# Performance work log

Measured on AMD Instinct MI355X. Metric: run time of the kernel, lower is better.

The kernel has to match this reference:

```python
import jax, jax.numpy as jnp
import numpy as np

# ---- config (from init_kwargs) ----
PRE_NMS_THRESH = 0.05
K = 200                    # pre_nms_top_n (fixed-size top-k for jit)
NUM_CLASSES = 80
FPN_STRIDE = 8
MASK_SCALE_FACTOR = 2
MASK_STRIDE = FPN_STRIDE / MASK_SCALE_FACTOR  # 4.0
IMG_H, IMG_W = 768, 768


def setup_inputs() -> dict:
    key = jax.random.key(0)
    ks = jax.random.split(key, 6)
    N, C, H, W, DIM = 2, NUM_CLASSES, 96, 96, 32
    # FCOS-style locations for the stride-8 level: center of each cell
    ys, xs = jnp.meshgrid(jnp.arange(H, dtype=jnp.float32),
                          jnp.arange(W, dtype=jnp.float32), indexing='ij')
    locations = jnp.stack([xs.reshape(-1), ys.reshape(-1)], axis=1) * FPN_STRIDE + FPN_STRIDE // 2
    return {
        'locations': locations,                                                 # [HW, 2]
        'box_cls': jax.random.normal(ks[0], (N, C, H, W), jnp.float32) - 2.0,   # mostly below thresh
        'box_regression': jax.random.uniform(ks[1], (N, 4, H, W), jnp.float32) * 100.0,
        'centerness': jax.random.normal(ks[2], (N, 1, H, W), jnp.float32),
        'proposal_embed': jax.random.normal(ks[3], (N, DIM, H, W), jnp.float32),
        'proposal_margin': jax.random.uniform(ks[4], (N, 1, H, W), jnp.float32, minval=0.1, maxval=2.0),
        'pixel_embed': jax.random.normal(ks[5], (N, DIM, 192, 192), jnp.float32),
    }


def reference(locations, box_cls, box_regression, centerness,
              proposal_embed, proposal_margin, pixel_embed):
    N, C, H, W = box_cls.shape
    DIM = proposal_embed.shape[1]
    o_h = pixel_embed.shape[2] * MASK_SCALE_FACTOR
    o_w = pixel_embed.shape[3] * MASK_SCALE_FACTOR

    # interpolate(pixel_embed, size=(o_h, o_w), mode='bilinear', align_corners=False)
    pix_up = jax.image.resize(pixel_embed, (N, DIM, o_h, o_w), method='bilinear')

    # NCHW -> [N, HW, C] flattening (matches permute(0,2,3,1).reshape)
    scores = jax.nn.sigmoid(jnp.transpose(box_cls.reshape(N, C, H * W), (0, 2, 1)))   # [N, HW, C]
    ctr = jax.nn.sigmoid(centerness.reshape(N, H * W))                                # [N, HW]
    reg = jnp.transpose(box_regression.reshape(N, 4, H * W), (0, 2, 1))               # [N, HW, 4]
    emb = jnp.transpose(proposal_embed.reshape(N, DIM, H * W), (0, 2, 1))             # [N, HW, DIM]
    mar = proposal_margin.reshape(N, H * W)                                           # [N, HW]

    xs = jnp.arange(o_w, dtype=jnp.float32)
    ys = jnp.arange(o_h, dtype=jnp.float32)

    def per_image(s, c, r, e, m, pix):
        # threshold + centerness-weighted score; invalid candidates rank last
        cand = s > PRE_NMS_THRESH                       # [HW, C]
        sc = s * c[:, None]                             # [HW, C]
        flat = jnp.where(cand, sc, -1.0).reshape(-1)    # [HW*C]
        topv, topi = jax.lax.top_k(flat, K)             # fixed-size top-k
        loc_idx = topi // C                             # [K]
        labels = topi % C + 1                           # [K]
        valid = topv > 0.0                              # padded slots when < K candidates

        # box decode: [x - l, y - t, x + r, y + b], clipped to image
        loc = locations[loc_idx]                        # [K, 2]
        rr = r[loc_idx]                                 # [K, 4]
        x1 = jnp.clip(loc[:, 0] - rr[:, 0], 0.0, IMG_W - 1)
        y1 = jnp.clip(loc[:, 1] - rr[:, 1], 0.0, IMG_H - 1)
        x2 = jnp.clip(loc[:, 0] + rr[:, 2], 0.0, IMG_W - 1)
        y2 = jnp.clip(loc[:, 1] + rr[:, 3], 0.0, IMG_H - 1)
        boxes = jnp.stack([x1, y1, x2, y2], axis=1)     # [K, 4]

        # boxes_to_masks at mask stride: binary inside-box masks [K, o_h, o_w]
        mb = boxes / MASK_STRIDE
        in_x = (xs[None, :] >= mb[:, 0:1]) & (xs[None, :] <= mb[:, 2:3])  # [K, o_w]
        in_y = (ys[None, :] >= mb[:, 1:2]) & (ys[None, :] <= mb[:, 3:4])  # [K, o_h]
        box_mask = in_y[:, :, None] & in_x[:, None, :]

        # pixel-embed distance mask: exp(-||pix - e_k||^2 * margin_k)
        ek = e[loc_idx]                                 # [K, DIM]
        mk = m[loc_idx]                                 # [K]
        p = pix.reshape(DIM, o_h * o_w)                 # [DIM, P]
        d2 = (jnp.sum(ek * ek, axis=1)[:, None]
              + jnp.sum(p * p, axis=0)[None, :]
              - 2.0 * ek @ p)                           # [K, P] via GEMM
        prob = jnp.exp(-d2 * mk[:, None]).reshape(K, o_h, o_w)
        masks = prob * box_mask.astype(prob.dtype) * valid[:, None, None].astype(prob.dtype)
        return masks

    masks = jax.vmap(per_image)(scores, ctr, reg, emb, mar, pix_up)  # [N, K, o_h, o_w]
    return masks
```

## Files before the change

kernel.cpp:

```cpp
#include <hip/hip_runtime.h>
#include <cmath>


namespace {
constexpr int NIMG = 2;
constexpr int NC   = 80;
constexpr int NHW  = 96 * 96;
constexpr int NCHW = NC * NHW;
constexpr int NDIM = 32;
constexpr int PH = 192, PW = 192;
constexpr int OH = 384, OW = 384;
constexpr int KTOP = 200;
constexpr int CAP = 4096;
constexpr int MCAP = 1024;
constexpr float PRE_THRESH = 0.05f;
constexpr unsigned KEY_ZERO = 0x80000000u;
constexpr float IMG_MAX = 767.0f;

constexpr int ZTILES = 6;
constexpr int NZB = NIMG * KTOP * ZTILES;

constexpr int NF4 = NCHW / 4;
constexpr int SEL_BLOCKS = 128;
constexpr int SEL_STRIDE = SEL_BLOCKS * 256;
constexpr int SEL_ITERS = (NF4 + SEL_STRIDE - 1) / SEL_STRIDE;
constexpr int LCAP = 512;

constexpr int WS_HIST1  = 0;
constexpr int WS_CNT    = WS_HIST1 + NIMG * 2048;
constexpr int WS_PAIRS  = 4104;
constexpr int WS_PARAMS = WS_PAIRS + NIMG * CAP * 2;
constexpr int PARAM_WORDS = 40;
constexpr int WS_ZERO_WORDS = WS_CNT + NIMG;

typedef float f4 __attribute__((ext_vector_type(4)));
}

__device__ __forceinline__ unsigned key_of(float f) {
  unsigned u = __float_as_uint(f);
  return (u & 0x80000000u) ? ~u : (u | 0x80000000u);
}

__device__ void scan2048(const unsigned* __restrict__ gh, int kwant,
                         unsigned* sh_cnt, unsigned* sh_sum, int* sh_bk,
                         int& b_out, int& kr_out) {
  const int t = threadIdx.x;
  __syncthreads();
  if (t == 0) { sh_bk[0] = -1; sh_bk[1] = kwant; }
  unsigned local = 0;
  for (int j = 0; j < 8; ++j) { unsigned v = gh[t * 8 + j]; sh_cnt[t * 8 + j] = v; local += v; }
  sh_sum[t] = local;
  __syncthreads();
  unsigned S = 0;
  for (int j = t + 1; j < 256; ++j) S += sh_sum[j];
  int cand_b = -1;
  unsigned cand_above = 0;
  unsigned run = S;
  for (int j = 7; j >= 0; --j) {
    const unsigned cv = sh_cnt[t * 8 + j];
    if (cand_b < 0 && run + cv >= (unsigned)kwant) { cand_b = t * 8 + j; cand_above = run; }
    run += cv;
  }
  if (cand_b >= 0) atomicMax(&sh_bk[0], cand_b);
  __syncthreads();
  if (cand_b >= 0 && cand_b == sh_bk[0]) sh_bk[1] = kwant - (int)cand_above;
  __syncthreads();
  b_out = (sh_bk[0] < 0) ? 0 : sh_bk[0];
  kr_out = sh_bk[1];
}

__global__ __launch_bounds__(256) void k_zero_ws(unsigned* __restrict__ ws) {
  const int i = blockIdx.x * 256 + threadIdx.x;
  for (int j = i; j < WS_ZERO_WORDS; j += 8 * 256) ws[j] = 0u;
}

__global__ __launch_bounds__(256) void k_keygen(const float* __restrict__ box_cls,
                                                const float* __restrict__ ctrness,
                                                unsigned* __restrict__ ws,
                                                uint4* __restrict__ keys) {
  __shared__ unsigned hist[2048];
  for (int i = threadIdx.x; i < 2048; i += 256) hist[i] = 0;
  __syncthreads();
  const int n = blockIdx.x >= SEL_BLOCKS;
  const int bi = blockIdx.x - n * SEL_BLOCKS;
  const float* cls = box_cls + n * NCHW;
  const float* ctr = ctrness + n * NHW;
  uint4* mykeys = keys + n * NF4;
  for (int s = 0; s < SEL_ITERS; ++s) {
    const int j4 = s * SEL_STRIDE + bi * 256 + threadIdx.x;
    if (j4 >= NF4) break;
    const int j = j4 * 4;
    const int c = j / NHW;
    const int hw = j - c * NHW;
    const f4 xv = *reinterpret_cast<const f4*>(cls + j);
    const f4 cv = *reinterpret_cast<const f4*>(ctr + hw);
    unsigned kk[4];
    #pragma unroll
    for (int q = 0; q < 4; ++q) {
      const float sg = 1.0f / (1.0f + expf(-xv[q]));
      float v = -1.0f;
      if (sg > PRE_THRESH) v = sg * (1.0f / (1.0f + expf(-cv[q])));
      const unsigned k = key_of(v);
      kk[q] = k;
      if (k > KEY_ZERO) atomicAdd(&hist[k >> 21], 1u);
    }
    mykeys[j4] = make_uint4(kk[0], kk[1], kk[2], kk[3]);
  }
  __syncthreads();
  unsigned* gh = ws + WS_HIST1 + n * 2048;
  for (int t = threadIdx.x; t < 2048; t += 256) { unsigned v = hist[t]; if (v) atomicAdd(&gh[t], v); }
}

__global__ __launch_bounds__(256) void k_gather(const uint4* __restrict__ keys,
                                                unsigned* __restrict__ ws) {
  __shared__ unsigned sh_cnt[2048];
  __shared__ unsigned sh_sum[256];
  __shared__ int sh_bk[2];
  __shared__ unsigned loc[LCAP][2];
  __shared__ int lcnt;
  __shared__ unsigned gbase;
  const int n = blockIdx.x >= SEL_BLOCKS;
  const int bi = blockIdx.x - n * SEL_BLOCKS;
  int b1i, kr;
  scan2048(ws + WS_HIST1 + n * 2048, KTOP, sh_cnt, sh_sum, sh_bk, b1i, kr);
  if (threadIdx.x == 0) lcnt = 0;
  __syncthreads();
  const unsigned b1 = (unsigned)b1i;
  const uint4* mykeys = keys + n * NF4;
  for (int s = 0; s < SEL_ITERS; ++s) {
    const int j4 = s * SEL_STRIDE + bi * 256 + threadIdx.x;
    if (j4 >= NF4) break;
    const uint4 kv = mykeys[j4];
    const unsigned kk[4] = {kv.x, kv.y, kv.z, kv.w};
    #pragma unroll
    for (int q = 0; q < 4; ++q) {
      if ((kk[q] >> 21) < b1) continue;
      const int j = j4 * 4 + q;
      const int c = j / NHW;
      const int hw = j - c * NHW;
      const int p = atomicAdd(&lcnt, 1);
      if (p < LCAP) { loc[p][0] = kk[q]; loc[p][1] = (unsigned)(hw * NC + c); }
    }
  }
  __syncthreads();
  const int lc = min(lcnt, LCAP);
  if (threadIdx.x == 0) gbase = atomicAdd(ws + WS_CNT + n, (unsigned)lc);
  __syncthreads();
  const unsigned gb = gbase;
  for (int i = threadIdx.x; i < lc; i += 256) {
    const unsigned pos = gb + (unsigned)i;
    if (pos < (unsigned)CAP) {
      ws[WS_PAIRS + (n * CAP + (int)pos) * 2]     = loc[i][0];
      ws[WS_PAIRS + (n * CAP + (int)pos) * 2 + 1] = loc[i][1];
    }
  }
}

__global__ __launch_bounds__(256) void k_final(unsigned* __restrict__ ws,
                                               const float* __restrict__ locations,
                                               const float* __restrict__ box_reg,
                                               const float* __restrict__ pemb,
                                               const float* __restrict__ pmar) {
  const int n = blockIdx.x;
  const int t = threadIdx.x;
  __shared__ unsigned sh_cnt[2048];
  __shared__ unsigned sh_sum[256];
  __shared__ int sh_bk[2];
  __shared__ uint2 P[CAP];
  __shared__ unsigned h256[256];
  __shared__ unsigned mKey[MCAP], mRef[MCAP];
  __shared__ int sh_b, sh_t;
  for (int s = t; s < KTOP; s += 256) ws[WS_PARAMS + (n * KTOP + s) * PARAM_WORDS] = 0u;
  int b1i, krem;
  scan2048(ws + WS_HIST1 + n * 2048, KTOP, sh_cnt, sh_sum, sh_bk, b1i, krem);
  const unsigned b1 = (unsigned)b1i;
  const int cnt = min((int)ws[WS_CNT + n], CAP);
  for (int i = t; i < cnt; i += 256) {
    P[i].x = ws[WS_PAIRS + (n * CAP + i) * 2];
    P[i].y = ws[WS_PAIRS + (n * CAP + i) * 2 + 1];
  }
  __syncthreads();

  unsigned prefix = b1;
  int shift = 21;
  #pragma unroll
  for (int level = 0; level < 2; ++level) {
    const int newshift = shift - 8;
    h256[t] = 0;
    if (t == 0) sh_b = 0;
    __syncthreads();
    for (int i = t; i < cnt; i += 256) {
      const unsigned k = P[i].x;
      if ((k >> shift) == prefix) atomicAdd(&h256[(k >> newshift) & 255u], 1u);
    }
    __syncthreads();
    const unsigned hv = h256[t];
    unsigned S = 0;
    for (int j = t + 1; j < 256; ++j) S += h256[j];
    if (S + hv >= (unsigned)krem) atomicMax(&sh_b, t);
    __syncthreads();
    const int b = sh_b;
    if (t == b) sh_t = krem - (int)S;
    __syncthreads();
    krem = sh_t;
    prefix = (prefix << 8) | (unsigned)b;
    shift = newshift;
    __syncthreads();
  }

  if (t == 0) sh_t = 0;
  __syncthreads();
  for (int i = t; i < cnt; i += 256) {
    const unsigned k = P[i].x;
    if ((k >> 5) >= prefix) {
      const int pos = atomicAdd(&sh_t, 1);
      if (pos < MCAP) { mKey[pos] = k; mRef[pos] = P[i].y; }
    }
  }
  __syncthreads();
  const int m = min(sh_t, MCAP);

  for (int i = t; i < m; i += 256) {
    const unsigned ki = mKey[i], ri = mRef[i];
    int rank = 0;
    for (int j = 0; j < m; ++j) {
      const unsigned kj = mKey[j], rj = mRef[j];
      rank += (kj > ki || (kj == ki && rj < ri)) ? 1 : 0;
    }
    if (rank >= KTOP) continue;
    unsigned* pp = ws + WS_PARAMS + (n * KTOP + rank) * PARAM_WORDS;
    int valid = 0;
    if (ki > KEY_ZERO) {
      const int hw = (int)ri / NC;
      const float lx = locations[2 * hw], ly = locations[2 * hw + 1];
      const float rl = box_reg[(n * 4 + 0) * NHW + hw];
      const float rt = box_reg[(n * 4 + 1) * NHW + hw];
      const float rr = box_reg[(n * 4 + 2) * NHW + hw];
      const float rb = box_reg[(n * 4 + 3) * NHW + hw];
      const float x1 = fminf(fmaxf(lx - rl, 0.f), IMG_MAX);
      const float y1 = fminf(fmaxf(ly - rt, 0.f), IMG_MAX);
      const float x2 = fminf(fmaxf(lx + rr, 0.f), IMG_MAX);
      const float y2 = fminf(fmaxf(ly + rb, 0.f), IMG_MAX);
      const int ix0 = max(0, (int)ceilf(x1 * 0.25f));
      const int ix1 = min(OW - 1, (int)floorf(x2 * 0.25f));
      const int iy0 = max(0, (int)ceilf(y1 * 0.25f));
      const int iy1 = min(OH - 1, (int)floorf(y2 * 0.25f));
      if (ix0 <= ix1 && iy0 <= iy1) {
        valid = 1;
        pp[1] = (unsigned)ix0; pp[2] = (unsigned)ix1;
        pp[3] = (unsigned)iy0; pp[4] = (unsigned)iy1;
        reinterpret_cast<float*>(pp)[5] = pmar[n * NHW + hw];
        float* ep = reinterpret_cast<float*>(pp) + 8;
        #pragma unroll
        for (int d = 0; d < NDIM; ++d) ep[d] = pemb[(n * NDIM + d) * NHW + hw];
      }
    }
    pp[0] = (unsigned)valid;
  }
}

__global__ __launch_bounds__(256) void k_out(const float* __restrict__ pix,
                                             const unsigned* __restrict__ ws,
                                             float* __restrict__ out) {
  const int bid = blockIdx.x;
  const int t = threadIdx.x;
  if (bid < NZB) {
    const int nk = bid / ZTILES;
    const int rt = bid - nk * ZTILES;
    const int y0 = rt * 64;
    const unsigned* meta = ws + WS_PARAMS + nk * PARAM_WORDS;
    f4* ob4 = reinterpret_cast<f4*>(out + (size_t)nk * (OH * OW)) + y0 * (OW / 4);
    const f4 z = {0.f, 0.f, 0.f, 0.f};
    int qa = 0, qb = -1, iy0 = 0, iy1 = -1;
    bool overlap = false;
    if (meta[0]) {
      iy0 = (int)meta[3]; iy1 = (int)meta[4];
      if (iy1 >= y0 && iy0 < y0 + 64) {
        overlap = true;
        qa = (int)meta[1] >> 2;
        qb = (int)meta[2] >> 2;
      }
    }
    if (!overlap) {
      #pragma unroll
      for (int i = 0; i < 24; ++i) ob4[i * 256 + t] = z;
    } else {
      for (int i = 0; i < 24; ++i) {
        const int idx = i * 256 + t;
        const int y = y0 + idx / 96;
        const int q = idx - (idx / 96) * 96;
        if (y >= iy0 && y <= iy1 && q >= qa && q <= qb) continue;
        ob4[idx] = z;
      }
    }
    return;
  }

  const int nk = bid - NZB;
  const unsigned* meta = ws + WS_PARAMS + nk * PARAM_WORDS;
  if (meta[0] == 0u) return;
  const int ix0 = (int)meta[1], ix1 = (int)meta[2];
  const int iy0 = (int)meta[3], iy1 = (int)meta[4];
  const int xp0 = (ix0 >> 2) << 2;
  const int xp1 = (ix1 >> 2) * 4 + 3;
  const float margin = __uint_as_float(meta[5]);
  float e[NDIM];
  {
    const float4* e4 = reinterpret_cast<const float4*>(meta + 8);
    #pragma unroll
    for (int q = 0; q < NDIM / 4; ++q) {
      const float4 v = e4[q];
      e[4 * q + 0] = v.x; e[4 * q + 1] = v.y; e[4 * q + 2] = v.z; e[4 * q + 3] = v.w;
    }
  }
  const int n = nk / KTOP;
  const float* peb = pix + (size_t)n * NDIM * PH * PW;
  float* ob = out + (size_t)nk * (OH * OW);

  const int tx = t & 63;
  const int ts = t >> 6;
  const int h = iy1 - iy0 + 1;
  const int shh = (h + 3) >> 2;
  const int ybeg = iy0 + ts * shh;
  const int yend = min(iy0 + (ts + 1) * shh, iy1 + 1);

  for (int c = xp0 + tx; c <= xp1; c += 64) {
    const bool inx = (c >= ix0) && (c <= ix1);
    const float sx = 0.5f * (float)c - 0.25f;
    const float xf = floorf(sx);
    const float fx = sx - xf;
    const int xs0 = max((int)xf, 0);
    const int xs1 = min((int)xf + 1, PW - 1);
    float qa_[NDIM], qb_[NDIM];
    int ra = -9, rb = -9;
    for (int y = ybeg; y < yend; ++y) {
      float val = 0.f;
      if (inx) {
        const float sy = 0.5f * (float)y - 0.25f;
        const float yf = floorf(sy);
        const float fy = sy - yf;
        const int ys0 = max((int)yf, 0);
        const int ys1 = min((int)yf + 1, PH - 1);
        if (ys0 != ra) {
          if (ys0 == rb) {
            #pragma unroll
            for (int d = 0; d < NDIM; ++d) qa_[d] = qb_[d];
          } else {
            const float* p = peb + (size_t)ys0 * PW;
            #pragma unroll
            for (int d = 0; d < NDIM; ++d)
              qa_[d] = (1.f - fx) * p[d * PH * PW + xs0] + fx * p[d * PH * PW + xs1];
          }
          ra = ys0;
        }
        if (ys1 != rb) {
          if (ys1 == ra) {
            #pragma unroll
            for (int d = 0; d < NDIM; ++d) qb_[d] = qa_[d];
          } else {
            const float* p = peb + (size_t)ys1 * PW;
            #pragma unroll
            for (int d = 0; d < NDIM; ++d)
              qb_[d] = (1.f - fx) * p[d * PH * PW + xs0] + fx * p[d * PH * PW + xs1];
          }
          rb = ys1;
        }
        float d2 = 0.f;
        #pragma unroll
        for (int d = 0; d < NDIM; ++d) {
          const float pv = qa_[d] + fy * (qb_[d] - qa_[d]);
          const float df = e[d] - pv;
          d2 = fmaf(df, df, d2);
        }
        val = expf(-d2 * margin);
      }
      ob[(size_t)y * OW + c] = val;
    }
  }
}

extern "C" void kernel_launch(void* const* d_in, const int* in_sizes, int n_in,
                              void* d_out, int out_size, void* d_ws, size_t ws_size,
                              hipStream_t stream) {
  const float* locations = (const float*)d_in[0];
  const float* box_cls   = (const float*)d_in[1];
  const float* box_reg   = (const float*)d_in[2];
  const float* ctrness   = (const float*)d_in[3];
  const float* pemb      = (const float*)d_in[4];
  const float* pmar      = (const float*)d_in[5];
  const float* pix       = (const float*)d_in[6];
  float* out = (float*)d_out;
  unsigned* ws = (unsigned*)d_ws;
  uint4* keys = (uint4*)d_out;

  k_zero_ws<<<dim3(8), dim3(256), 0, stream>>>(ws);
  k_keygen <<<dim3(2 * SEL_BLOCKS), dim3(256), 0, stream>>>(box_cls, ctrness, ws, keys);
  k_gather <<<dim3(2 * SEL_BLOCKS), dim3(256), 0, stream>>>(keys, ws);
  k_final  <<<dim3(NIMG), dim3(256), 0, stream>>>(ws, locations, box_reg, pemb, pmar);
  k_out    <<<dim3(NZB + NIMG * KTOP), dim3(256), 0, stream>>>(pix, ws, out);
}
```

Before: 108.0 us.

## Fuse keygen, gather and final selection into one kernel with grid barrier

Merges the three selection kernels into a single persistent kernel. Score keys stay in registers instead of round-tripping through the output buffer. A global atomic spin barrier now separates the histogram from the gather, and a last-block ticket runs the final top-k and parameter packing. This removes two launches and the key store/reload, but relies on all 256 blocks being co-resident for the spin barrier. The output kernel is also reordered so the per-box compute blocks launch before the zero-fill blocks.

```diff
diff --git a/kernel.cpp b/kernel.cpp
--- a/kernel.cpp
+++ b/kernel.cpp
@@ -13,25 +13,28 @@
 constexpr int KTOP = 200;
 constexpr int CAP = 4096;
 constexpr int MCAP = 1024;
+constexpr int LCAP = 512;
 constexpr float PRE_THRESH = 0.05f;
 constexpr unsigned KEY_ZERO = 0x80000000u;
 constexpr float IMG_MAX = 767.0f;
 
+constexpr int NBOX = NIMG * KTOP;
 constexpr int ZTILES = 6;
-constexpr int NZB = NIMG * KTOP * ZTILES;
+constexpr int NZB = NBOX * ZTILES;
 
 constexpr int NF4 = NCHW / 4;
 constexpr int SEL_BLOCKS = 128;
 constexpr int SEL_STRIDE = SEL_BLOCKS * 256;
 constexpr int SEL_ITERS = (NF4 + SEL_STRIDE - 1) / SEL_STRIDE;
-constexpr int LCAP = 512;
 
 constexpr int WS_HIST1  = 0;
 constexpr int WS_CNT    = WS_HIST1 + NIMG * 2048;
+constexpr int WS_BAR    = WS_CNT + NIMG;
+constexpr int WS_TICK   = WS_BAR + 1;
+constexpr int WS_ZERO_WORDS = WS_TICK + NIMG;
 constexpr int WS_PAIRS  = 4104;
 constexpr int WS_PARAMS = WS_PAIRS + NIMG * CAP * 2;
 constexpr int PARAM_WORDS = 40;
-constexpr int WS_ZERO_WORDS = WS_CNT + NIMG;
 
 typedef float f4 __attribute__((ext_vector_type(4)));
 }
@@ -41,143 +44,146 @@
   return (u & 0x80000000u) ? ~u : (u | 0x80000000u);
 }
 
-__device__ void scan2048(const unsigned* __restrict__ gh, int kwant,
-                         unsigned* sh_cnt, unsigned* sh_sum, int* sh_bk,
-                         int& b_out, int& kr_out) {
-  const int t = threadIdx.x;
-  __syncthreads();
-  if (t == 0) { sh_bk[0] = -1; sh_bk[1] = kwant; }
-  unsigned local = 0;
-  for (int j = 0; j < 8; ++j) { unsigned v = gh[t * 8 + j]; sh_cnt[t * 8 + j] = v; local += v; }
-  sh_sum[t] = local;
-  __syncthreads();
-  unsigned S = 0;
-  for (int j = t + 1; j < 256; ++j) S += sh_sum[j];
-  int cand_b = -1;
-  unsigned cand_above = 0;
-  unsigned run = S;
-  for (int j = 7; j >= 0; --j) {
-    const unsigned cv = sh_cnt[t * 8 + j];
-    if (cand_b < 0 && run + cv >= (unsigned)kwant) { cand_b = t * 8 + j; cand_above = run; }
-    run += cv;
-  }
-  if (cand_b >= 0) atomicMax(&sh_bk[0], cand_b);
-  __syncthreads();
-  if (cand_b >= 0 && cand_b == sh_bk[0]) sh_bk[1] = kwant - (int)cand_above;
-  __syncthreads();
-  b_out = (sh_bk[0] < 0) ? 0 : sh_bk[0];
-  kr_out = sh_bk[1];
-}
-
 __global__ __launch_bounds__(256) void k_zero_ws(unsigned* __restrict__ ws) {
-  const int i = blockIdx.x * 256 + threadIdx.x;
-  for (int j = i; j < WS_ZERO_WORDS; j += 8 * 256) ws[j] = 0u;
-}
-
-__global__ __launch_bounds__(256) void k_keygen(const float* __restrict__ box_cls,
-                                                const float* __restrict__ ctrness,
-                                                unsigned* __restrict__ ws,
-                                                uint4* __restrict__ keys) {
+  for (int j = threadIdx.x; j < WS_ZERO_WORDS; j += 256) ws[j] = 0u;
+}
+
+__global__ __launch_bounds__(256) void k_select(
+    const float* __restrict__ box_cls, const float* __restrict__ ctrness,
+    const float* __restrict__ locations, const float* __restrict__ box_reg,
+    const float* __restrict__ pemb, const float* __restrict__ pmar,
+    unsigned* __restrict__ ws) {
   __shared__ unsigned hist[2048];
-  for (int i = threadIdx.x; i < 2048; i += 256) hist[i] = 0;
-  __syncthreads();
-  const int n = blockIdx.x >= SEL_BLOCKS;
-  const int bi = blockIdx.x - n * SEL_BLOCKS;
-  const float* cls = box_cls + n * NCHW;
-  const float* ctr = ctrness + n * NHW;
-  uint4* mykeys = keys + n * NF4;
-  for (int s = 0; s < SEL_ITERS; ++s) {
-    const int j4 = s * SEL_STRIDE + bi * 256 + threadIdx.x;
-    if (j4 >= NF4) break;
-    const int j = j4 * 4;
-    const int c = j / NHW;
-    const int hw = j - c * NHW;
-    const f4 xv = *reinterpret_cast<const f4*>(cls + j);
-    const f4 cv = *reinterpret_cast<const f4*>(ctr + hw);
-    unsigned kk[4];
-    #pragma unroll
-    for (int q = 0; q < 4; ++q) {
-      const float sg = 1.0f / (1.0f + expf(-xv[q]));
-      float v = -1.0f;
-      if (sg > PRE_THRESH) v = sg * (1.0f / (1.0f + expf(-cv[q])));
-      const unsigned k = key_of(v);
-      kk[q] = k;
-      if (k > KEY_ZERO) atomicAdd(&hist[k >> 21], 1u);
-    }
-    mykeys[j4] = make_uint4(kk[0], kk[1], kk[2], kk[3]);
-  }
-  __syncthreads();
-  unsigned* gh = ws + WS_HIST1 + n * 2048;
-  for (int t = threadIdx.x; t < 2048; t += 256) { unsigned v = hist[t]; if (v) atomicAdd(&gh[t], v); }
-}
-
-__global__ __launch_bounds__(256) void k_gather(const uint4* __restrict__ keys,
-                                                unsigned* __restrict__ ws) {
-  __shared__ unsigned sh_cnt[2048];
   __shared__ unsigned sh_sum[256];
   __shared__ int sh_bk[2];
   __shared__ unsigned loc[LCAP][2];
   __shared__ int lcnt;
   __shared__ unsigned gbase;
+  __shared__ int sh_last;
+  const int t = threadIdx.x;
   const int n = blockIdx.x >= SEL_BLOCKS;
   const int bi = blockIdx.x - n * SEL_BLOCKS;
-  int b1i, kr;
-  scan2048(ws + WS_HIST1 + n * 2048, KTOP, sh_cnt, sh_sum, sh_bk, b1i, kr);
-  if (threadIdx.x == 0) lcnt = 0;
-  __syncthreads();
-  const unsigned b1 = (unsigned)b1i;
-  const uint4* mykeys = keys + n * NF4;
+
+  for (int i = t; i < 2048; i += 256) hist[i] = 0;
+  __syncthreads();
+  const float* cls = box_cls + n * NCHW;
+  const float* ctr = ctrness + n * NHW;
+  unsigned kk[SEL_ITERS][4];
+  #pragma unroll
   for (int s = 0; s < SEL_ITERS; ++s) {
-    const int j4 = s * SEL_STRIDE + bi * 256 + threadIdx.x;
-    if (j4 >= NF4) break;
-    const uint4 kv = mykeys[j4];
-    const unsigned kk[4] = {kv.x, kv.y, kv.z, kv.w};
+    const int j4 = s * SEL_STRIDE + bi * 256 + t;
+    if (j4 < NF4) {
+      const int j = j4 * 4;
+      const int c = j / NHW;
+      const int hw = j - c * NHW;
+      const f4 xv = *reinterpret_cast<const f4*>(cls + j);
+      const f4 cv = *reinterpret_cast<const f4*>(ctr + hw);
+      #pragma unroll
+      for (int q = 0; q < 4; ++q) {
+        const float sg = 1.0f / (1.0f + expf(-xv[q]));
+        float v = -1.0f;
+        if (sg > PRE_THRESH) v = sg * (1.0f / (1.0f + expf(-cv[q])));
+        const unsigned k = key_of(v);
+        kk[s][q] = k;
+        if (k > KEY_ZERO) atomicAdd(&hist[k >> 21], 1u);
+      }
+    } else {
+      #pragma unroll
+      for (int q = 0; q < 4; ++q) kk[s][q] = 0u;
+    }
+  }
+  __syncthreads();
+  {
+    unsigned* gh = ws + WS_HIST1 + n * 2048;
+    for (int i = t; i < 2048; i += 256) { unsigned v = hist[i]; if (v) atomicAdd(&gh[i], v); }
+  }
+
+  __syncthreads();
+  if (t == 0) {
+    atomicAdd(ws + WS_BAR, 1u);
+    while (__hip_atomic_load(ws + WS_BAR, __ATOMIC_RELAXED,
+                             __HIP_MEMORY_SCOPE_AGENT) < (unsigned)(2 * SEL_BLOCKS)) {
+      __builtin_amdgcn_s_sleep(2);
+    }
+  }
+  __syncthreads();
+
+  if (t == 0) { sh_bk[0] = -1; sh_bk[1] = KTOP; }
+  {
+    const unsigned* gh = ws + WS_HIST1 + n * 2048;
+    unsigned local = 0;
+    for (int j = 0; j < 8; ++j) { unsigned v = gh[t * 8 + j]; hist[t * 8 + j] = v; local += v; }
+    sh_sum[t] = local;
+  }
+  __syncthreads();
+  {
+    unsigned S = 0;
+    for (int j = t + 1; j < 256; ++j) S += sh_sum[j];
+    int cand_b = -1;
+    unsigned cand_above = 0;
+    unsigned run = S;
+    for (int j = 7; j >= 0; --j) {
+      const unsigned cv = hist[t * 8 + j];
+      if (cand_b < 0 && run + cv >= (unsigned)KTOP) { cand_b = t * 8 + j; cand_above = run; }
+      run += cv;
+    }
+    if (cand_b >= 0) atomicMax(&sh_bk[0], cand_b);
+    __syncthreads();
+    if (cand_b >= 0 && cand_b == sh_bk[0]) sh_bk[1] = KTOP - (int)cand_above;
+    __syncthreads();
+  }
+  const unsigned b1 = (unsigned)(sh_bk[0] < 0 ? 0 : sh_bk[0]);
+  int krem = sh_bk[1];
+
+  if (t == 0) lcnt = 0;
+  __syncthreads();
+  #pragma unroll
+  for (int s = 0; s < SEL_ITERS; ++s) {
     #pragma unroll
     for (int q = 0; q < 4; ++q) {
-      if ((kk[q] >> 21) < b1) continue;
-      const int j = j4 * 4 + q;
+      const unsigned k = kk[s][q];
+      if ((k >> 21) < b1) continue;
+      const int j = (s * SEL_STRIDE + bi * 256 + t) * 4 + q;
       const int c = j / NHW;
       const int hw = j - c * NHW;
       const int p = atomicAdd(&lcnt, 1);
-      if (p < LCAP) { loc[p][0] = kk[q]; loc[p][1] = (unsigned)(hw * NC + c); }
+      if (p < LCAP) { loc[p][0] = k; loc[p][1] = (unsigned)(hw * NC + c); }
     }
   }
   __syncthreads();
   const int lc = min(lcnt, LCAP);
-  if (threadIdx.x == 0) gbase = atomicAdd(ws + WS_CNT + n, (unsigned)lc);
-  __syncthreads();
-  const unsigned gb = gbase;
-  for (int i = threadIdx.x; i < lc; i += 256) {
-    const unsigned pos = gb + (unsigned)i;
+  if (t == 0) gbase = atomicAdd(ws + WS_CNT + n, (unsigned)lc);
+  __syncthreads();
+  for (int i = t; i < lc; i += 256) {
+    const unsigned pos = gbase + (unsigned)i;
     if (pos < (unsigned)CAP) {
-      ws[WS_PAIRS + (n * CAP + (int)pos) * 2]     = loc[i][0];
-      ws[WS_PAIRS + (n * CAP + (int)pos) * 2 + 1] = loc[i][1];
-    }
-  }
-}
-
-__global__ __launch_bounds__(256) void k_final(unsigned* __restrict__ ws,
-                                               const float* __restrict__ locations,
-                                               const float* __restrict__ box_reg,
-                                               const float* __restrict__ pemb,
-                                               const float* __restrict__ pmar) {
-  const int n = blockIdx.x;
-  const int t = threadIdx.x;
-  __shared__ unsigned sh_cnt[2048];
-  __shared__ unsigned sh_sum[256];
-  __shared__ int sh_bk[2];
+      __hip_atomic_store(&ws[WS_PAIRS + (n * CAP + (int)pos) * 2], loc[i][0],
+                         __ATOMIC_RELAXED, __HIP_MEMORY_SCOPE_AGENT);
+      __hip_atomic_store(&ws[WS_PAIRS + (n * CAP + (int)pos) * 2 + 1], loc[i][1],
+                         __ATOMIC_RELAXED, __HIP_MEMORY_SCOPE_AGENT);
+    }
+  }
+
+  __syncthreads();
+  if (t == 0) {
+    const unsigned old = atomicAdd(ws + WS_TICK + n, 1u);
+    sh_last = (old == (unsigned)(SEL_BLOCKS - 1)) ? 1 : 0;
+  }
+  __syncthreads();
+  if (!sh_last) return;
+
   __shared__ uint2 P[CAP];
   __shared__ unsigned h256[256];
   __shared__ unsigned mKey[MCAP], mRef[MCAP];
   __shared__ int sh_b, sh_t;
   for (int s = t; s < KTOP; s += 256) ws[WS_PARAMS + (n * KTOP + s) * PARAM_WORDS] = 0u;
-  int b1i, krem;
-  scan2048(ws + WS_HIST1 + n * 2048, KTOP, sh_cnt, sh_sum, sh_bk, b1i, krem);
-  const unsigned b1 = (unsigned)b1i;
-  const int cnt = min((int)ws[WS_CNT + n], CAP);
+  const int cnt = min((int)__hip_atomic_load(ws + WS_CNT + n, __ATOMIC_RELAXED,
+                                             __HIP_MEMORY_SCOPE_AGENT), CAP);
   for (int i = t; i < cnt; i += 256) {
-    P[i].x = ws[WS_PAIRS + (n * CAP + i) * 2];
-    P[i].y = ws[WS_PAIRS + (n * CAP + i) * 2 + 1];
+    P[i].x = __hip_atomic_load(&ws[WS_PAIRS + (n * CAP + i) * 2],
+                               __ATOMIC_RELAXED, __HIP_MEMORY_SCOPE_AGENT);
+    P[i].y = __hip_atomic_load(&ws[WS_PAIRS + (n * CAP + i) * 2 + 1],
+                               __ATOMIC_RELAXED, __HIP_MEMORY_SCOPE_AGENT);
   }
   __syncthreads();
 
@@ -264,9 +270,10 @@
                                              float* __restrict__ out) {
   const int bid = blockIdx.x;
   const int t = threadIdx.x;
-  if (bid < NZB) {
-    const int nk = bid / ZTILES;
-    const int rt = bid - nk * ZTILES;
+  if (bid >= NBOX) {
+    const int zb = bid - NBOX;
+    const int nk = zb / ZTILES;
+    const int rt = zb - nk * ZTILES;
     const int y0 = rt * 64;
     const unsigned* meta = ws + WS_PARAMS + nk * PARAM_WORDS;
     f4* ob4 = reinterpret_cast<f4*>(out + (size_t)nk * (OH * OW)) + y0 * (OW / 4);
@@ -296,7 +303,7 @@
     return;
   }
 
-  const int nk = bid - NZB;
+  const int nk = bid;
   const unsigned* meta = ws + WS_PARAMS + nk * PARAM_WORDS;
   if (meta[0] == 0u) return;
   const int ix0 = (int)meta[1], ix1 = (int)meta[2];
@@ -391,11 +398,9 @@
   const float* pix       = (const float*)d_in[6];
   float* out = (float*)d_out;
   unsigned* ws = (unsigned*)d_ws;
-  uint4* keys = (uint4*)d_out;
-
-  k_zero_ws<<<dim3(8), dim3(256), 0, stream>>>(ws);
-  k_keygen <<<dim3(2 * SEL_BLOCKS), dim3(256), 0, stream>>>(box_cls, ctrness, ws, keys);
-  k_gather <<<dim3(2 * SEL_BLOCKS), dim3(256), 0, stream>>>(keys, ws);
-  k_final  <<<dim3(NIMG), dim3(256), 0, stream>>>(ws, locations, box_reg, pemb, pmar);
-  k_out    <<<dim3(NZB + NIMG * KTOP), dim3(256), 0, stream>>>(pix, ws, out);
-}
+
+  k_zero_ws<<<dim3(1), dim3(256), 0, stream>>>(ws);
+  k_select <<<dim3(2 * SEL_BLOCKS), dim3(256), 0, stream>>>(
+      box_cls, ctrness, locations, box_reg, pemb, pmar, ws);
+  k_out    <<<dim3(NBOX + NZB), dim3(256), 0, stream>>>(pix, ws, out);
+}
```

Result: faster. 100.8 us (median of 2 runs) (-6.6%).
